# Kernel optimization log

Hardware: AMD Instinct MI355X
Metric: run time of the kernel (lower is better)

The kernel has to match this reference:

```python
import jax, jax.numpy as jnp
import numpy as np
import math

D_MODEL = 1024
NUM_HEADS = 16
D_K = D_MODEL // NUM_HEADS


def setup_inputs() -> dict:
    key = jax.random.key(0)
    ks = jax.random.split(key, 7)
    B, S = 2, 2048
    scale = 1.0 / math.sqrt(D_MODEL)
    inp = {
        "q": jax.random.normal(ks[0], (B, S, D_MODEL), dtype=jnp.float32),
        "k": jax.random.normal(ks[1], (B, S, D_MODEL), dtype=jnp.float32),
        "v": jax.random.normal(ks[2], (B, S, D_MODEL), dtype=jnp.float32),
        # Source module reuses q_linear for q, k, and v projections, so only
        # Wq/bq are needed for the input projections; out projection separate.
        "Wq": jax.random.normal(ks[3], (D_MODEL, D_MODEL), dtype=jnp.float32) * scale,
        "bq": jnp.zeros((D_MODEL,), dtype=jnp.float32),
        "Wo": jax.random.normal(ks[4], (D_MODEL, D_MODEL), dtype=jnp.float32) * scale,
        "bo": jnp.zeros((D_MODEL,), dtype=jnp.float32),
    }
    return inp


def _attention(q, k, v, Wq, bq, Wo, bo):
    B, S, _ = q.shape

    def proj(x):
        # [B,S,D] -> [B,H,S,d_k]
        y = jnp.einsum("bsd,de->bse", x, Wq) + bq
        return y.reshape(B, S, NUM_HEADS, D_K).transpose(0, 2, 1, 3)

    qh, kh, vh = proj(q), proj(k), proj(v)
    # scores: [B,H,S,S]
    scores = jnp.einsum("bhsd,bhtd->bhst", qh, kh) / math.sqrt(D_K)
    attn = jax.nn.softmax(scores, axis=-1)
    # dropout: eval-mode identity
    out = jnp.einsum("bhst,bhtd->bhsd", attn, vh)  # [B,H,S,d_k]
    out = out.transpose(0, 2, 1, 3).reshape(B, S, D_MODEL)
    return jnp.einsum("bsd,de->bse", out, Wo) + bo


def reference(q, k, v, Wq, bq, Wo, bo):
    return _attention(q, k, v, Wq, bq, Wo, bo)
```

## Files before the change

kernel.cpp:

```cpp
#include <hip/hip_runtime.h>
#include <hip/hip_bf16.h>

typedef unsigned short u16;
typedef unsigned int   u32;
typedef __attribute__((ext_vector_type(8))) short bf16x8;
typedef __attribute__((ext_vector_type(4))) float f32x4;
typedef __attribute__((ext_vector_type(16))) float f32x16;

#define SEQ     2048
#define DM      1024
#define NH      16
#define DKH     64
#define PER_SRC 4194304

#define OFF_VT   0u
#define OFF_AOH  8388608u
#define OFF_WQT  25165824u
#define OFF_WOT  27262976u
#define OFF_QH   29360128u
#define OFF_KH   37748736u
#define OFF_VH   46137344u
#define OFF_PO   54525952u
#define OFF_PML  88080384u
#define NEED_WS  89128960u
#define PART_O_F 4194304
#define PART_ML_F 131072

__device__ __forceinline__ u16 f2bf(float f) {
    union { float f; u32 u; } c; c.f = f;
    return (u16)((c.u + 0x7fffu + ((c.u >> 16) & 1u)) >> 16);
}

__device__ __forceinline__ u32 cvt_pk_bf16(float lo, float hi) {
    u32 r;
    asm("v_cvt_pk_bf16_f32 %0, %1, %2" : "=v"(r) : "v"(lo), "v"(hi));
    return r;
}

__device__ __forceinline__ void gload_lds16(const void* g, void* l) {
    __builtin_amdgcn_global_load_lds((__attribute__((address_space(1))) void*)g,
                                     (__attribute__((address_space(3))) void*)l,
                                     16, 0, 0);
}

__global__ void cast_qkv(const float* __restrict__ q, const float* __restrict__ k,
                         const float* __restrict__ v, u16* __restrict__ xb) {
    const float* src = (blockIdx.y == 0) ? q : (blockIdx.y == 1) ? k : v;
    u16* dst = xb + (size_t)blockIdx.y * PER_SRC;
    size_t i = ((size_t)blockIdx.x * 256 + threadIdx.x) * 8;
    float4 a = *(const float4*)(src + i);
    float4 b = *(const float4*)(src + i + 4);
    bf16x8 o;
    o[0] = (short)f2bf(a.x); o[1] = (short)f2bf(a.y);
    o[2] = (short)f2bf(a.z); o[3] = (short)f2bf(a.w);
    o[4] = (short)f2bf(b.x); o[5] = (short)f2bf(b.y);
    o[6] = (short)f2bf(b.z); o[7] = (short)f2bf(b.w);
    *(bf16x8*)(dst + i) = o;
}

__global__ void wtrans(const float* __restrict__ Wq, const float* __restrict__ Wo,
                       u16* __restrict__ Wqt, u16* __restrict__ Wot) {
    const float* W = blockIdx.y ? Wo : Wq;
    u16* Wt       = blockIdx.y ? Wot : Wqt;
    int k0 = (blockIdx.x & 15) * 64;
    int n0 = (blockIdx.x >> 4) * 64;
    __shared__ __align__(16) float t[64][68];
    int tid = threadIdx.x;
    int r = tid >> 2, cs = (tid & 3) * 16;
    #pragma unroll
    for (int j = 0; j < 4; ++j) {
        float4 vv = *(const float4*)(W + (size_t)(k0 + r) * DM + n0 + cs + j * 4);
        *(float4*)&t[r][cs + j * 4] = vv;
    }
    __syncthreads();
    bf16x8 o0, o1;
    #pragma unroll
    for (int j = 0; j < 8; ++j) o0[j] = (short)f2bf(t[cs + j][r]);
    #pragma unroll
    for (int j = 0; j < 8; ++j) o1[j] = (short)f2bf(t[cs + 8 + j][r]);
    u16* dst = Wt + (size_t)(n0 + r) * DM + k0 + cs;
    *(bf16x8*)(dst)     = o0;
    *(bf16x8*)(dst + 8) = o1;
}

__global__ void vtrans(const u16* __restrict__ vh, u16* __restrict__ vt) {
    int bh = blockIdx.y, st = blockIdx.x;
    __shared__ u16 t[64][72];
    int tid = threadIdx.x;
    int r = tid >> 2, cs = (tid & 3) * 16;
    const u16* src = vh + ((size_t)bh * SEQ + st * 64 + r) * DKH + cs;
    bf16x8 v0 = *(const bf16x8*)(src);
    bf16x8 v1 = *(const bf16x8*)(src + 8);
    #pragma unroll
    for (int j = 0; j < 8; ++j) { t[r][cs + j] = (u16)v0[j]; t[r][cs + 8 + j] = (u16)v1[j]; }
    __syncthreads();
    bf16x8 o0, o1;
    #pragma unroll
    for (int j = 0; j < 8; ++j) o0[j] = (short)t[cs + j][r];
    #pragma unroll
    for (int j = 0; j < 8; ++j) o1[j] = (short)t[cs + 8 + j][r];
    bf16x8 w0, w1;
    #pragma unroll
    for (int j = 0; j < 4; ++j) {
        w0[j] = o0[j];     w0[4 + j] = o1[j];
        w1[j] = o0[4 + j]; w1[4 + j] = o1[4 + j];
    }
    u16* dst = vt + ((size_t)bh * DKH + r) * SEQ + st * 64 + cs;
    *(bf16x8*)(dst)     = w0;
    *(bf16x8*)(dst + 8) = w1;
}

template<int MODE>
__global__ __launch_bounds__(256)
void gemm_bt(const u16* __restrict__ Abase, const u16* __restrict__ Bt,
             const float* __restrict__ bias, void* __restrict__ outbase)
{
    __shared__ __align__(16) u16 Alds[128 * 64];
    __shared__ __align__(16) u16 Blds[128 * 64];

    const int tid  = threadIdx.x;
    const int wave = tid >> 6;
    const int lane = tid & 63;
    const int low4 = lane & 15;
    const int quad = lane >> 4;
    const int bid  = blockIdx.x;
    const int xcd  = bid & 7;
    const int j    = bid >> 3;
    const int m0 = (xcd * 4 + (j >> 3)) * 128;
    const int n0 = (j & 7) * 128;
    const int wm = (wave >> 1) * 64, wn = (wave & 1) * 64;

    const u16* A = Abase + (size_t)blockIdx.z * PER_SRC;

    f32x4 acc[4][4] = {};

    for (int kt = 0; kt < DM / 64; ++kt) {
        #pragma unroll
        for (int it = 0; it < 4; ++it) {
            int seg  = it * 256 + tid;
            int row  = seg >> 3;
            int slot = seg & 7;
            int ss   = slot ^ (row & 7);
            const u16* srcA;
            if (MODE == 0) {
                srcA = A + (size_t)(m0 + row) * DM + kt * 64 + ss * 8;
            } else {
                int m = m0 + row;
                srcA = A + (((size_t)((m >> 11) * NH + kt)) * SEQ + (m & (SEQ - 1))) * DKH + ss * 8;
            }
            gload_lds16(srcA, &Alds[(it * 256 + wave * 64) * 8]);
            gload_lds16(Bt + (size_t)(n0 + row) * DM + kt * 64 + ss * 8,
                        &Blds[(it * 256 + wave * 64) * 8]);
        }
        __syncthreads();
        #pragma unroll
        for (int kk = 0; kk < 2; ++kk) {
            bf16x8 af[4], bfr[4];
            #pragma unroll
            for (int mi = 0; mi < 4; ++mi) {
                int row = wm + mi * 16 + low4;
                af[mi] = *(const bf16x8*)&Alds[row * 64 + (((kk * 4 + quad) ^ (row & 7)) * 8)];
            }
            #pragma unroll
            for (int ni = 0; ni < 4; ++ni) {
                int row = wn + ni * 16 + low4;
                bfr[ni] = *(const bf16x8*)&Blds[row * 64 + (((kk * 4 + quad) ^ (row & 7)) * 8)];
            }
            #pragma unroll
            for (int mi = 0; mi < 4; ++mi)
                #pragma unroll
                for (int ni = 0; ni < 4; ++ni)
                    acc[mi][ni] = __builtin_amdgcn_mfma_f32_16x16x32_bf16(
                        af[mi], bfr[ni], acc[mi][ni], 0, 0, 0);
        }
        __syncthreads();
    }

    #pragma unroll
    for (int mi = 0; mi < 4; ++mi) {
        #pragma unroll
        for (int ni = 0; ni < 4; ++ni) {
            int n = n0 + wn + ni * 16 + low4;
            float bv = bias[n];
            #pragma unroll
            for (int j2 = 0; j2 < 4; ++j2) {
                int m = m0 + wm + mi * 16 + quad * 4 + j2;
                float val = acc[mi][ni][j2] + bv;
                if (MODE == 0) {
                    u16* dst = (u16*)outbase + (size_t)blockIdx.z * PER_SRC;
                    int b = m >> 11, s = m & (SEQ - 1);
                    int h = n >> 6, dd = n & 63;
                    dst[(size_t)(b * NH + h) * (SEQ * DKH) + (size_t)s * DKH + dd] = f2bf(val);
                } else {
                    ((float*)outbase)[(size_t)m * DM + n] = val;
                }
            }
        }
    }
}

template<int SPLIT>
__global__ __launch_bounds__(256, 2)
void attn(const u16* __restrict__ qh, const u16* __restrict__ kh,
          const u16* __restrict__ vt, u16* __restrict__ aoh,
          float* __restrict__ pO, float* __restrict__ pml)
{
    __shared__ __align__(16) u16 lds[2][8192];

    const int tid  = threadIdx.x;
    const int w    = tid >> 6;
    const int lane = tid & 63;
    const int l31  = lane & 31;
    const int hi   = lane >> 5;

    int bid = blockIdx.x;
    int lid = (bid & 7) * 64 + (bid >> 3);
    const int qt = lid & 15;
    const int bh = lid >> 4;
    const int part = SPLIT ? blockIdx.y : 0;
    const int kt0  = part * 16;
    const int nkt  = SPLIT ? 16 : 32;

    const int qbase = qt * 128 + w * 32;
    const int q_row = qbase + l31;

    const float SC = 0.18033688f;

    bf16x8 qf[4];
    #pragma unroll
    for (int c = 0; c < 4; ++c)
        qf[c] = *(const bf16x8*)&qh[((size_t)bh * SEQ + q_row) * DKH + c * 16 + hi * 8];

    float m_r = -1e30f, l_r = 0.f;
    f32x16 ot[2] = {};

#define STAGE(buf, kt_)                                                                 \
    {                                                                                   \
        _Pragma("unroll")                                                               \
        for (int it = 0; it < 2; ++it) {                                                \
            int seg  = it * 256 + tid;                                                  \
            int row  = seg >> 3;                                                        \
            int slot = seg & 7;                                                         \
            int ss   = slot ^ (row & 7);                                                \
            gload_lds16(kh + ((size_t)bh * SEQ + (kt_) * 64 + row) * DKH + ss * 8,      \
                        &lds[buf][(it * 256 + w * 64) * 8]);                            \
            gload_lds16(vt + ((size_t)bh * DKH + row) * SEQ + (kt_) * 64 + ss * 8,      \
                        &lds[buf][4096 + (it * 256 + w * 64) * 8]);                     \
        }                                                                               \
    }

    STAGE(0, kt0);
    __syncthreads();

    int cur = 0;
    for (int ki = 0; ki < nkt; ++ki) {
        if (ki + 1 < nkt) STAGE(cur ^ 1, kt0 + ki + 1);

        const u16* Klds = &lds[cur][0];
        const u16* Vlds = &lds[cur][4096];

        f32x16 st[2];
        #pragma unroll
        for (int T = 0; T < 2; ++T) {
            f32x16 acc = {};
            __builtin_amdgcn_s_setprio(1);
            #pragma unroll
            for (int c = 0; c < 4; ++c) {
                int row = T * 32 + l31;
                bf16x8 kf = *(const bf16x8*)&Klds[row * 64 + (((c * 2 + hi) ^ (row & 7)) * 8)];
                acc = __builtin_amdgcn_mfma_f32_32x32x16_bf16(kf, qf[c], acc, 0, 0, 0);
            }
            __builtin_amdgcn_s_setprio(0);
            st[T] = acc;
        }

        float mx[8];
        #pragma unroll
        for (int r = 0; r < 8; ++r)
            mx[r] = fmaxf(fmaxf(st[0][r], st[0][r + 8]),
                          fmaxf(st[1][r], st[1][r + 8]));
        float t0 = fmaxf(fmaxf(mx[0], mx[1]), mx[2]);
        float t1 = fmaxf(fmaxf(mx[3], mx[4]), mx[5]);
        float t2 = fmaxf(mx[6], mx[7]);
        float lmax = fmaxf(fmaxf(t0, t1), t2);
        float mloc = fmaxf(lmax, __shfl_xor(lmax, 32)) * SC;

        float mnew = fmaxf(m_r, mloc);
        if (!__all(mloc <= m_r + 11.5f)) {
            float fac = __builtin_amdgcn_exp2f(m_r - mnew);
            m_r = mnew;
            l_r *= fac;
            #pragma unroll
            for (int dt = 0; dt < 2; ++dt)
                #pragma unroll
                for (int r = 0; r < 16; ++r) ot[dt][r] *= fac;
        }

        float nm = -m_r;
        float rs0 = 0.f, rs1 = 0.f, rs2 = 0.f, rs3 = 0.f;
        #pragma unroll
        for (int T = 0; T < 2; ++T)
            #pragma unroll
            for (int r = 0; r < 16; r += 4) {
                float p0 = __builtin_amdgcn_exp2f(fmaf(st[T][r],     SC, nm));
                float p1 = __builtin_amdgcn_exp2f(fmaf(st[T][r + 1], SC, nm));
                float p2 = __builtin_amdgcn_exp2f(fmaf(st[T][r + 2], SC, nm));
                float p3 = __builtin_amdgcn_exp2f(fmaf(st[T][r + 3], SC, nm));
                st[T][r] = p0; st[T][r + 1] = p1; st[T][r + 2] = p2; st[T][r + 3] = p3;
                rs0 += p0; rs1 += p1; rs2 += p2; rs3 += p3;
            }
        float rsum = (rs0 + rs1) + (rs2 + rs3);
        l_r += rsum + __shfl_xor(rsum, 32);

        u32 pk[2][8];
        #pragma unroll
        for (int T = 0; T < 2; ++T)
            #pragma unroll
            for (int g = 0; g < 8; ++g)
                pk[T][g] = cvt_pk_bf16(st[T][2 * g], st[T][2 * g + 1]);

        __builtin_amdgcn_s_setprio(1);
        #pragma unroll
        for (int dt = 0; dt < 2; ++dt)
            #pragma unroll
            for (int c = 0; c < 4; ++c) {
                int row = dt * 32 + l31;
                bf16x8 vf = *(const bf16x8*)&Vlds[row * 64 + (((c * 2 + hi) ^ (row & 7)) * 8)];
                union { bf16x8 v; u32 u[4]; } pf;
                int T = c >> 1, g0 = (c & 1) * 4;
                pf.u[0] = pk[T][g0];     pf.u[1] = pk[T][g0 + 1];
                pf.u[2] = pk[T][g0 + 2]; pf.u[3] = pk[T][g0 + 3];
                ot[dt] = __builtin_amdgcn_mfma_f32_32x32x16_bf16(vf, pf.v, ot[dt], 0, 0, 0);
            }
        __builtin_amdgcn_s_setprio(0);

        __syncthreads();
        cur ^= 1;
    }

    if (SPLIT == 0) {
        float inv = 1.0f / l_r;
        u16* tile = &lds[0][0] + w * 2048;
        #pragma unroll
        for (int dt = 0; dt < 2; ++dt)
            #pragma unroll
            for (int g = 0; g < 4; ++g) {
                u32 w0 = cvt_pk_bf16(ot[dt][4 * g] * inv,     ot[dt][4 * g + 1] * inv);
                u32 w1 = cvt_pk_bf16(ot[dt][4 * g + 2] * inv, ot[dt][4 * g + 3] * inv);
                int d0 = 8 * g + 4 * hi + 32 * dt;
                int byteoff = l31 * 128 + ((d0 * 2) ^ ((l31 & 7) << 4));
                uint2 pr; pr.x = w0; pr.y = w1;
                *(uint2*)((char*)tile + byteoff) = pr;
            }
        const size_t gbase = ((size_t)bh * SEQ + qbase) * DKH;
        #pragma unroll
        for (int p = 0; p < 4; ++p) {
            int q = p * 8 + (lane >> 3);
            int byteoff = q * 128 + (((lane & 7) * 16) ^ ((q & 7) << 4));
            bf16x8 val = *(const bf16x8*)((const char*)tile + byteoff);
            *(bf16x8*)&aoh[gbase + p * 512 + lane * 8] = val;
        }
    } else {
        float* ftile = (float*)&lds[0][0] + w * 2048;
        #pragma unroll
        for (int dt = 0; dt < 2; ++dt)
            #pragma unroll
            for (int g = 0; g < 4; ++g) {
                int d0 = 8 * g + 4 * hi + 32 * dt;
                int slot = (d0 >> 2) ^ (l31 & 15);
                f32x4 vv;
                vv[0] = ot[dt][4 * g];     vv[1] = ot[dt][4 * g + 1];
                vv[2] = ot[dt][4 * g + 2]; vv[3] = ot[dt][4 * g + 3];
                *(f32x4*)((char*)ftile + l31 * 256 + slot * 16) = vv;
            }
        float* po = pO + (size_t)part * PART_O_F + ((size_t)bh * SEQ + qbase) * DKH;
        #pragma unroll
        for (int p = 0; p < 8; ++p) {
            int q = p * 4 + (lane >> 4);
            int chunk = lane & 15;
            f32x4 val = *(const f32x4*)((const char*)ftile + q * 256 + ((chunk ^ (q & 15)) * 16));
            *(f32x4*)&po[(size_t)q * DKH + chunk * 4] = val;
        }
        if (hi == 0) {
            float2 ml; ml.x = m_r; ml.y = l_r;
            *(float2*)&pml[(size_t)part * PART_ML_F + ((size_t)bh * SEQ + qbase + l31) * 2] = ml;
        }
    }
#undef STAGE
}

__global__ __launch_bounds__(256)
void attn_merge(const float* __restrict__ pO, const float* __restrict__ pml,
                u16* __restrict__ aoh)
{
    int tid = threadIdx.x;
    int bh = blockIdx.x >> 5;
    int qb = blockIdx.x & 31;
    int ql = tid >> 2;
    int dc = tid & 3;
    size_t row = (size_t)bh * SEQ + qb * 64 + ql;

    float2 ml1 = *(const float2*)&pml[row * 2];
    float2 ml2 = *(const float2*)&pml[PART_ML_F + row * 2];
    float m  = fmaxf(ml1.x, ml2.x);
    float w1 = __builtin_amdgcn_exp2f(ml1.x - m);
    float w2 = __builtin_amdgcn_exp2f(ml2.x - m);
    float inv = 1.0f / (ml1.y * w1 + ml2.y * w2);
    float a1 = w1 * inv, a2 = w2 * inv;

    const f32x4* r1 = (const f32x4*)&pO[row * DKH + dc * 16];
    const f32x4* r2 = (const f32x4*)&pO[PART_O_F + row * DKH + dc * 16];
    u16* dst = aoh + row * DKH + dc * 16;
    u16 outv[16];
    #pragma unroll
    for (int i = 0; i < 4; ++i) {
        f32x4 x = r1[i], y = r2[i];
        #pragma unroll
        for (int j = 0; j < 4; ++j)
            outv[i * 4 + j] = f2bf(x[j] * a1 + y[j] * a2);
    }
    *(bf16x8*)(dst)     = *(bf16x8*)&outv[0];
    *(bf16x8*)(dst + 8) = *(bf16x8*)&outv[8];
}

extern "C" void kernel_launch(void* const* d_in, const int* in_sizes, int n_in,
                              void* d_out, int out_size, void* d_ws, size_t ws_size,
                              hipStream_t stream)
{
    const float* q  = (const float*)d_in[0];
    const float* k  = (const float*)d_in[1];
    const float* v  = (const float*)d_in[2];
    const float* Wq = (const float*)d_in[3];
    const float* bq = (const float*)d_in[4];
    const float* Wo = (const float*)d_in[5];
    const float* bo = (const float*)d_in[6];

    char* ws = (char*)d_ws;
    u16* xb  = (u16*)(ws);
    u16* wqt = (u16*)(ws + OFF_WQT);
    u16* wot = (u16*)(ws + OFF_WOT);
    u16* qh  = (u16*)(ws + OFF_QH);
    u16* kh  = (u16*)(ws + OFF_KH);
    u16* vh  = (u16*)(ws + OFF_VH);
    u16* vt  = (u16*)(ws + OFF_VT);
    u16* aoh = (u16*)(ws + OFF_AOH);
    float* pO  = (float*)(ws + OFF_PO);
    float* pml = (float*)(ws + OFF_PML);

    cast_qkv<<<dim3(2048, 3), dim3(256), 0, stream>>>(q, k, v, xb);
    wtrans<<<dim3(256, 2), dim3(256), 0, stream>>>(Wq, Wo, wqt, wot);
    gemm_bt<0><<<dim3(256, 1, 3), dim3(256), 0, stream>>>(xb, wqt, bq, (void*)qh);
    vtrans<<<dim3(32, 32), dim3(256), 0, stream>>>(vh, vt);
    if (ws_size >= (size_t)NEED_WS) {
        attn<1><<<dim3(512, 2), dim3(256), 0, stream>>>(qh, kh, vt, aoh, pO, pml);
        attn_merge<<<dim3(1024), dim3(256), 0, stream>>>(pO, pml, aoh);
    } else {
        attn<0><<<dim3(512), dim3(256), 0, stream>>>(qh, kh, vt, aoh, pO, pml);
    }
    gemm_bt<1><<<dim3(256), dim3(256), 0, stream>>>(aoh, wot, bo, d_out);
}
```

Measured before the change: 140.9 us.

## Split attention KV into four parts and store partial outputs in bf16

```diff
diff --git a/kernel.cpp b/kernel.cpp
--- a/kernel.cpp
+++ b/kernel.cpp
@@ -20,15 +20,20 @@
 #define OFF_QH   29360128u
 #define OFF_KH   37748736u
 #define OFF_VH   46137344u
+#define OFF_PML  46137344u
 #define OFF_PO   54525952u
-#define OFF_PML  88080384u
-#define NEED_WS  89128960u
-#define PART_O_F 4194304
+#define NEED_WS  88080384u
+#define PART_O_U 4194304
 #define PART_ML_F 131072
 
 __device__ __forceinline__ u16 f2bf(float f) {
     union { float f; u32 u; } c; c.f = f;
     return (u16)((c.u + 0x7fffu + ((c.u >> 16) & 1u)) >> 16);
+}
+
+__device__ __forceinline__ float bf2f(u16 h) {
+    union { u32 u; float f; } c; c.u = (u32)h << 16;
+    return c.f;
 }
 
 __device__ __forceinline__ u32 cvt_pk_bf16(float lo, float hi) {
@@ -203,7 +208,7 @@
 __global__ __launch_bounds__(256, 2)
 void attn(const u16* __restrict__ qh, const u16* __restrict__ kh,
           const u16* __restrict__ vt, u16* __restrict__ aoh,
-          float* __restrict__ pO, float* __restrict__ pml)
+          u16* __restrict__ pOb, float* __restrict__ pml)
 {
     __shared__ __align__(16) u16 lds[2][8192];
 
@@ -218,8 +223,8 @@
     const int qt = lid & 15;
     const int bh = lid >> 4;
     const int part = SPLIT ? blockIdx.y : 0;
-    const int kt0  = part * 16;
-    const int nkt  = SPLIT ? 16 : 32;
+    const int kt0  = SPLIT ? part * 8 : 0;
+    const int nkt  = SPLIT ? 8 : 32;
 
     const int qbase = qt * 128 + w * 32;
     const int q_row = qbase + l31;
@@ -338,59 +343,37 @@
         cur ^= 1;
     }
 
-    if (SPLIT == 0) {
-        float inv = 1.0f / l_r;
-        u16* tile = &lds[0][0] + w * 2048;
-        #pragma unroll
-        for (int dt = 0; dt < 2; ++dt)
-            #pragma unroll
-            for (int g = 0; g < 4; ++g) {
-                u32 w0 = cvt_pk_bf16(ot[dt][4 * g] * inv,     ot[dt][4 * g + 1] * inv);
-                u32 w1 = cvt_pk_bf16(ot[dt][4 * g + 2] * inv, ot[dt][4 * g + 3] * inv);
-                int d0 = 8 * g + 4 * hi + 32 * dt;
-                int byteoff = l31 * 128 + ((d0 * 2) ^ ((l31 & 7) << 4));
-                uint2 pr; pr.x = w0; pr.y = w1;
-                *(uint2*)((char*)tile + byteoff) = pr;
-            }
-        const size_t gbase = ((size_t)bh * SEQ + qbase) * DKH;
-        #pragma unroll
-        for (int p = 0; p < 4; ++p) {
-            int q = p * 8 + (lane >> 3);
-            int byteoff = q * 128 + (((lane & 7) * 16) ^ ((q & 7) << 4));
-            bf16x8 val = *(const bf16x8*)((const char*)tile + byteoff);
-            *(bf16x8*)&aoh[gbase + p * 512 + lane * 8] = val;
-        }
-    } else {
-        float* ftile = (float*)&lds[0][0] + w * 2048;
-        #pragma unroll
-        for (int dt = 0; dt < 2; ++dt)
-            #pragma unroll
-            for (int g = 0; g < 4; ++g) {
-                int d0 = 8 * g + 4 * hi + 32 * dt;
-                int slot = (d0 >> 2) ^ (l31 & 15);
-                f32x4 vv;
-                vv[0] = ot[dt][4 * g];     vv[1] = ot[dt][4 * g + 1];
-                vv[2] = ot[dt][4 * g + 2]; vv[3] = ot[dt][4 * g + 3];
-                *(f32x4*)((char*)ftile + l31 * 256 + slot * 16) = vv;
-            }
-        float* po = pO + (size_t)part * PART_O_F + ((size_t)bh * SEQ + qbase) * DKH;
-        #pragma unroll
-        for (int p = 0; p < 8; ++p) {
-            int q = p * 4 + (lane >> 4);
-            int chunk = lane & 15;
-            f32x4 val = *(const f32x4*)((const char*)ftile + q * 256 + ((chunk ^ (q & 15)) * 16));
-            *(f32x4*)&po[(size_t)q * DKH + chunk * 4] = val;
-        }
-        if (hi == 0) {
-            float2 ml; ml.x = m_r; ml.y = l_r;
-            *(float2*)&pml[(size_t)part * PART_ML_F + ((size_t)bh * SEQ + qbase + l31) * 2] = ml;
-        }
+    float inv = (SPLIT == 0) ? (1.0f / l_r) : 1.0f;
+    u16* dstb = (SPLIT == 0) ? aoh : (pOb + (size_t)part * PART_O_U);
+    u16* tile = &lds[0][0] + w * 2048;
+    #pragma unroll
+    for (int dt = 0; dt < 2; ++dt)
+        #pragma unroll
+        for (int g = 0; g < 4; ++g) {
+            u32 w0 = cvt_pk_bf16(ot[dt][4 * g] * inv,     ot[dt][4 * g + 1] * inv);
+            u32 w1 = cvt_pk_bf16(ot[dt][4 * g + 2] * inv, ot[dt][4 * g + 3] * inv);
+            int d0 = 8 * g + 4 * hi + 32 * dt;
+            int byteoff = l31 * 128 + ((d0 * 2) ^ ((l31 & 7) << 4));
+            uint2 pr; pr.x = w0; pr.y = w1;
+            *(uint2*)((char*)tile + byteoff) = pr;
+        }
+    const size_t gbase = ((size_t)bh * SEQ + qbase) * DKH;
+    #pragma unroll
+    for (int p = 0; p < 4; ++p) {
+        int q = p * 8 + (lane >> 3);
+        int byteoff = q * 128 + (((lane & 7) * 16) ^ ((q & 7) << 4));
+        bf16x8 val = *(const bf16x8*)((const char*)tile + byteoff);
+        *(bf16x8*)&dstb[gbase + p * 512 + lane * 8] = val;
+    }
+    if (SPLIT == 1 && hi == 0) {
+        float2 ml; ml.x = m_r; ml.y = l_r;
+        *(float2*)&pml[(size_t)part * PART_ML_F + ((size_t)bh * SEQ + qbase + l31) * 2] = ml;
     }
 #undef STAGE
 }
 
 __global__ __launch_bounds__(256)
-void attn_merge(const float* __restrict__ pO, const float* __restrict__ pml,
+void attn_merge(const u16* __restrict__ pOb, const float* __restrict__ pml,
                 u16* __restrict__ aoh)
 {
     int tid = threadIdx.x;
@@ -400,25 +383,40 @@
     int dc = tid & 3;
     size_t row = (size_t)bh * SEQ + qb * 64 + ql;
 
-    float2 ml1 = *(const float2*)&pml[row * 2];
-    float2 ml2 = *(const float2*)&pml[PART_ML_F + row * 2];
-    float m  = fmaxf(ml1.x, ml2.x);
-    float w1 = __builtin_amdgcn_exp2f(ml1.x - m);
-    float w2 = __builtin_amdgcn_exp2f(ml2.x - m);
-    float inv = 1.0f / (ml1.y * w1 + ml2.y * w2);
-    float a1 = w1 * inv, a2 = w2 * inv;
-
-    const f32x4* r1 = (const f32x4*)&pO[row * DKH + dc * 16];
-    const f32x4* r2 = (const f32x4*)&pO[PART_O_F + row * DKH + dc * 16];
+    float2 ml[4];
+    #pragma unroll
+    for (int p = 0; p < 4; ++p)
+        ml[p] = *(const float2*)&pml[(size_t)p * PART_ML_F + row * 2];
+    float m = fmaxf(fmaxf(ml[0].x, ml[1].x), fmaxf(ml[2].x, ml[3].x));
+    float wgt[4];
+    float denom = 0.f;
+    #pragma unroll
+    for (int p = 0; p < 4; ++p) {
+        wgt[p] = __builtin_amdgcn_exp2f(ml[p].x - m);
+        denom += wgt[p] * ml[p].y;
+    }
+    float invd = 1.0f / denom;
+    #pragma unroll
+    for (int p = 0; p < 4; ++p) wgt[p] *= invd;
+
+    float acc[16];
+    #pragma unroll
+    for (int i = 0; i < 16; ++i) acc[i] = 0.f;
+    #pragma unroll
+    for (int p = 0; p < 4; ++p) {
+        const u16* src = pOb + (size_t)p * PART_O_U + row * DKH + dc * 16;
+        bf16x8 x0 = *(const bf16x8*)(src);
+        bf16x8 x1 = *(const bf16x8*)(src + 8);
+        #pragma unroll
+        for (int i = 0; i < 8; ++i) {
+            acc[i]     = fmaf(bf2f((u16)x0[i]), wgt[p], acc[i]);
+            acc[8 + i] = fmaf(bf2f((u16)x1[i]), wgt[p], acc[8 + i]);
+        }
+    }
     u16* dst = aoh + row * DKH + dc * 16;
     u16 outv[16];
     #pragma unroll
-    for (int i = 0; i < 4; ++i) {
-        f32x4 x = r1[i], y = r2[i];
-        #pragma unroll
-        for (int j = 0; j < 4; ++j)
-            outv[i * 4 + j] = f2bf(x[j] * a1 + y[j] * a2);
-    }
+    for (int i = 0; i < 16; ++i) outv[i] = f2bf(acc[i]);
     *(bf16x8*)(dst)     = *(bf16x8*)&outv[0];
     *(bf16x8*)(dst + 8) = *(bf16x8*)&outv[8];
 }
@@ -444,7 +442,7 @@
     u16* vh  = (u16*)(ws + OFF_VH);
     u16* vt  = (u16*)(ws + OFF_VT);
     u16* aoh = (u16*)(ws + OFF_AOH);
-    float* pO  = (float*)(ws + OFF_PO);
+    u16* pOb = (u16*)(ws + OFF_PO);
     float* pml = (float*)(ws + OFF_PML);
 
     cast_qkv<<<dim3(2048, 3), dim3(256), 0, stream>>>(q, k, v, xb);
@@ -452,10 +450,10 @@
     gemm_bt<0><<<dim3(256, 1, 3), dim3(256), 0, stream>>>(xb, wqt, bq, (void*)qh);
     vtrans<<<dim3(32, 32), dim3(256), 0, stream>>>(vh, vt);
     if (ws_size >= (size_t)NEED_WS) {
-        attn<1><<<dim3(512, 2), dim3(256), 0, stream>>>(qh, kh, vt, aoh, pO, pml);
-        attn_merge<<<dim3(1024), dim3(256), 0, stream>>>(pO, pml, aoh);
+        attn<1><<<dim3(512, 4), dim3(256), 0, stream>>>(qh, kh, vt, aoh, pOb, pml);
+        attn_merge<<<dim3(1024), dim3(256), 0, stream>>>(pOb, pml, aoh);
     } else {
-        attn<0><<<dim3(512), dim3(256), 0, stream>>>(qh, kh, vt, aoh, pO, pml);
+        attn<0><<<dim3(512), dim3(256), 0, stream>>>(qh, kh, vt, aoh, pOb, pml);
     }
     gemm_bt<1><<<dim3(256), dim3(256), 0, stream>>>(aoh, wot, bo, d_out);
 }
```

After: 141.6 us. No clear change (+0.5%).
